# Performance work log

Measured on AMD Instinct MI355X. Metric: run time of the kernel, lower is better.

Reference implementation:

```python
import jax, jax.numpy as jnp
import numpy as np

NUM_USERS = 100000
NUM_ITEMS = 50000
EMBED_DIM = 64
NUM_LAYERS = 3
NUM_PAIRS = 2000000  # symmetrized -> 4M directed edges


def setup_inputs() -> dict:
    key = jax.random.key(0)
    k_u, k_i, k_eu, k_ei = jax.random.split(key, 4)
    # Xavier-uniform-ish embedding tables
    bound_u = float(np.sqrt(6.0 / (NUM_USERS + EMBED_DIM)))
    bound_i = float(np.sqrt(6.0 / (NUM_ITEMS + EMBED_DIM)))
    user_weight = jax.random.uniform(k_u, (NUM_USERS, EMBED_DIM), jnp.float32, -bound_u, bound_u)
    item_weight = jax.random.uniform(k_i, (NUM_ITEMS, EMBED_DIM), jnp.float32, -bound_i, bound_i)
    users = jax.random.randint(k_eu, (NUM_PAIRS,), 0, NUM_USERS)
    items = jax.random.randint(k_ei, (NUM_PAIRS,), 0, NUM_ITEMS) + NUM_USERS
    # symmetric bipartite graph: user->item and item->user
    row = jnp.concatenate([users, items])
    col = jnp.concatenate([items, users])
    edge_index = jnp.stack([row, col])  # [2, 4M]
    return {"edge_index": edge_index, "user_weight": user_weight, "item_weight": item_weight}


def _lightgcn_conv(x, row, col, num_nodes):
    # deg over target (col) nodes
    deg = jax.ops.segment_sum(jnp.ones_like(col, dtype=x.dtype), col, num_segments=num_nodes)
    deg_inv_sqrt = jnp.where(deg > 0, jax.lax.rsqrt(jnp.maximum(deg, 1)), 0.0).astype(x.dtype)
    norm = deg_inv_sqrt[row] * deg_inv_sqrt[col]          # [E]
    msg = norm[:, None] * x[row]                           # gather + scale, [E, d]
    return jax.ops.segment_sum(msg, col, num_segments=num_nodes)  # scatter-add


def reference(edge_index, user_weight, item_weight):
    num_nodes = NUM_USERS + NUM_ITEMS
    row, col = edge_index[0], edge_index[1]
    x = jnp.concatenate([user_weight, item_weight], axis=0)  # [N, d]
    acc = x
    for _ in range(NUM_LAYERS):
        x = _lightgcn_conv(x, row, col, num_nodes)
        acc = acc + x
    final = acc / (NUM_LAYERS + 1)  # mean over layer embeddings
    return final[:NUM_USERS], final[NUM_USERS:]
```

## Files before the change

kernel.cpp:

```cpp
#include <hip/hip_runtime.h>


#define MAXBUK 640
#define CHUNK 4096
#define MAXBE 12288

__device__ __forceinline__ ushort f2bf(float f) {
  union { float f; unsigned int i; } cv;
  cv.f = f;
  unsigned int u = cv.i + 0x7FFFu + ((cv.i >> 16) & 1u);
  return (ushort)(u >> 16);
}

__device__ __forceinline__ float bflo(unsigned int w) {
  union { unsigned int i; float f; } cv;
  cv.i = w << 16;
  return cv.f;
}

__device__ __forceinline__ float bfhi(unsigned int w) {
  union { unsigned int i; float f; } cv;
  cv.i = w & 0xFFFF0000u;
  return cv.f;
}

__device__ __forceinline__ int wave_incl_scan(int v) {
  int lane = threadIdx.x & 63;
#pragma unroll
  for (int off = 1; off < 64; off <<= 1) {
    int t = __shfl_up(v, off, 64);
    if (lane >= off) v += t;
  }
  return v;
}


__global__ __launch_bounds__(256) void bhist_k(const int4* __restrict__ col4, int E4,
                                               const int* __restrict__ col, int E,
                                               int* __restrict__ bcnt, int nbuk) {
  __shared__ int lc[MAXBUK];
  for (int b = threadIdx.x; b < nbuk; b += 256) lc[b] = 0;
  __syncthreads();
  int i = blockIdx.x * 256 + threadIdx.x;
  int stride = gridDim.x * 256;
  for (int j = i; j < E4; j += stride) {
    int4 c = col4[j];
    atomicAdd(&lc[c.x >> 8], 1);
    atomicAdd(&lc[c.y >> 8], 1);
    atomicAdd(&lc[c.z >> 8], 1);
    atomicAdd(&lc[c.w >> 8], 1);
  }
  for (int j = E4 * 4 + i; j < E; j += stride) atomicAdd(&lc[col[j] >> 8], 1);
  __syncthreads();
  for (int b = threadIdx.x; b < nbuk; b += 256) {
    int c = lc[b];
    if (c) atomicAdd(&bcnt[b], c);
  }
}


__global__ void bscan_k(const int* __restrict__ bcnt, int* __restrict__ boffs,
                        int* __restrict__ gcursor, ushort* __restrict__ za,
                        ushort* __restrict__ zb, int nbuk, int E, int N) {
  int tid = threadIdx.x;
  int v = (tid < nbuk) ? bcnt[tid] : 0;
  int incl = wave_incl_scan(v);
  __shared__ int wsum[16];
  int wid = tid >> 6, lane = tid & 63;
  if (lane == 63) wsum[wid] = incl;
  __syncthreads();
  if (tid == 0) {
    int run = 0;
#pragma unroll
    for (int j = 0; j < 16; ++j) { int t = wsum[j]; wsum[j] = run; run += t; }
  }
  __syncthreads();
  int excl = incl - v + wsum[wid];
  if (tid < nbuk) {
    boffs[tid] = excl;
    gcursor[tid] = excl;
  }
  if (tid == 0) boffs[nbuk] = E;
  if (tid < 64) {
    za[N * 64 + tid] = 0;
    zb[N * 64 + tid] = 0;
  }
}


__global__ __launch_bounds__(256) void part_k(
    const int* __restrict__ row, const int* __restrict__ col, int E,
    int* __restrict__ gcursor, int* __restrict__ ebk, int nbuk) {
  __shared__ int cnt[MAXBUK];
  __shared__ int start[MAXBUK];
  __shared__ int ghead[MAXBUK];
  __shared__ int ebuf[CHUNK];
  __shared__ int gofs[CHUNK];
  __shared__ int wsum[4];

  const int tid = threadIdx.x;
  const int base = blockIdx.x * CHUNK;
  const int m = min(CHUNK, E - base);

  for (int b = tid; b < nbuk; b += 256) cnt[b] = 0;
  __syncthreads();

  int rec[16];
  int bb[16];
#pragma unroll
  for (int k = 0; k < 16; ++k) {
    int idx = k * 256 + tid;
    bb[k] = -1;
    if (idx < m) {
      int i = base + idx;
      int c = col[i];
      int r = row[i];
      rec[k] = r | ((c & 255) << 18);
      bb[k] = c >> 8;
      atomicAdd(&cnt[c >> 8], 1);
    }
  }
  __syncthreads();

  const int b0 = tid * 3;
  int lc0 = (b0 + 0 < nbuk) ? cnt[b0 + 0] : 0;
  int lc1 = (b0 + 1 < nbuk) ? cnt[b0 + 1] : 0;
  int lc2 = (b0 + 2 < nbuk) ? cnt[b0 + 2] : 0;
  int s = lc0 + lc1 + lc2;
  int incl = wave_incl_scan(s);
  int wid = tid >> 6, lane = tid & 63;
  if (lane == 63) wsum[wid] = incl;
  __syncthreads();
  int wb = 0;
#pragma unroll
  for (int j = 0; j < 4; ++j)
    if (j < wid) wb += wsum[j];
  int run = incl - s + wb;
  if (b0 + 0 < nbuk) { start[b0 + 0] = run; run += lc0; }
  if (b0 + 1 < nbuk) { start[b0 + 1] = run; run += lc1; }
  if (b0 + 2 < nbuk) { start[b0 + 2] = run; run += lc2; }
  __syncthreads();

  for (int b = tid; b < nbuk; b += 256) {
    int cb = cnt[b];
    if (cb > 0) {
      int g = atomicAdd(&gcursor[b], cb);
      ghead[b] = g - start[b];
    }
  }
  __syncthreads();

#pragma unroll
  for (int k = 0; k < 16; ++k) {
    if (bb[k] >= 0) {
      int slot = atomicAdd(&start[bb[k]], 1);
      ebuf[slot] = rec[k];
      gofs[slot] = ghead[bb[k]];
    }
  }
  __syncthreads();

  for (int s2 = tid; s2 < m; s2 += 256) ebk[gofs[s2] + s2] = ebuf[s2];
}


__global__ __launch_bounds__(256) void bsort_k(
    const int* __restrict__ boffs, const int* __restrict__ ebk,
    int* __restrict__ srcs, int* __restrict__ offs,
    float* __restrict__ dis, float* __restrict__ dis2,
    const float4* __restrict__ uw4, const float4* __restrict__ iw4,
    ushort* __restrict__ za, int N, int NU, int E) {
  __shared__ int cnt[256];
  __shared__ float disv[256];
  __shared__ int wsum[4];
  __shared__ int obuf[MAXBE];
  const int tid = threadIdx.x;
  const int node0 = blockIdx.x << 8;
  const int nn = min(256, N - node0);
  const int g0 = boffs[blockIdx.x];
  const int g1 = boffs[blockIdx.x + 1];
  const int m = g1 - g0;

  cnt[tid] = 0;
  __syncthreads();
  for (int i = tid; i < m; i += 256) atomicAdd(&cnt[(ebk[g0 + i] >> 18) & 255], 1);
  __syncthreads();

  int v = cnt[tid];
  int incl = wave_incl_scan(v);
  int wid = tid >> 6, lane = tid & 63;
  if (lane == 63) wsum[wid] = incl;
  __syncthreads();
  int wb = 0;
#pragma unroll
  for (int j = 0; j < 4; ++j)
    if (j < wid) wb += wsum[j];
  int excl = incl - v + wb;

  float dv = v > 0 ? 1.0f / sqrtf((float)v) : 0.0f;
  disv[tid] = dv;
  if (tid < nn) {
    int node = node0 + tid;
    offs[node] = g0 + excl;
    dis[node] = dv;
    dis2[node] = dv * dv;
  }
  if (blockIdx.x == 0 && tid == 0) offs[N] = E;

  __syncthreads();
  cnt[tid] = excl;
  __syncthreads();

  for (int i = tid; i < m; i += 256) {
    int r = ebk[g0 + i];
    int slot = atomicAdd(&cnt[(r >> 18) & 255], 1);
    if (slot < MAXBE) obuf[slot] = r & 0x3FFFF;
  }
  __syncthreads();
  for (int i = tid; i < m; i += 256) srcs[g0 + i] = obuf[i];

  for (int g = tid; g < nn * 16; g += 256) {
    int rel = g >> 4;
    int comp = g & 15;
    int node = node0 + rel;
    float4 x = (node < NU) ? uw4[node * 16 + comp] : iw4[(node - NU) * 16 + comp];
    float d = disv[rel];
    ushort4 o;
    o.x = f2bf(x.x * d);
    o.y = f2bf(x.y * d);
    o.z = f2bf(x.z * d);
    o.w = f2bf(x.w * d);
    *reinterpret_cast<ushort4*>(&za[node * 64 + comp * 4]) = o;
  }
}


template <int LAYER>
__global__ __launch_bounds__(256) void spmm_k(
    const int* __restrict__ offs, const int* __restrict__ srcs,
    const ushort* __restrict__ zin, ushort* __restrict__ zout,
    const float* __restrict__ uw, const float* __restrict__ iw,
    const float* __restrict__ dis, const float* __restrict__ dis2,
    float* __restrict__ dout, int N, int NU) {
  int wid = blockIdx.x * 4 + (threadIdx.x >> 6);
  int lane = threadIdx.x & 63;
  if (wid >= N) return;
  int NI = N - NU;
  int n = (wid < NI) ? (NU + wid) : (wid - NI);
  n = __builtin_amdgcn_readfirstlane(n);
  int e0 = __builtin_amdgcn_readfirstlane(offs[n]);
  int e1 = __builtin_amdgcn_readfirstlane(offs[n + 1]);

  const int li = lane & 31;
  const int hi = lane >> 5;

  float ax = 0.0f, ay = 0.0f;
  for (int base = e0; base < e1; base += 64) {
    int rem = e1 - base;
    int src = (lane < rem) ? srcs[base + lane] : N;
    int kk = min(rem, 64);
    for (int j = 0; j < kk; j += 8) {
#pragma unroll
      for (int t = 0; t < 4; ++t) {
        int sA = __builtin_amdgcn_readlane(src, j + 2 * t);
        int sB = __builtin_amdgcn_readlane(src, j + 2 * t + 1);
        int s = hi ? sB : sA;
        unsigned int w32 =
            *reinterpret_cast<const unsigned int*>(&zin[(s << 6) + li * 2]);
        ax += bflo(w32);
        ay += bfhi(w32);
      }
    }
  }
  ax += __shfl_xor(ax, 32, 64);
  ay += __shfl_xor(ay, 32, 64);

  if (hi == 0) {
    float d1 = dis[n];
    int o = n * 64 + li * 2;
    float xlx = d1 * ax, xly = d1 * ay;
    if (LAYER == 1) {
      const float* xp = (n < NU) ? (uw + o) : (iw + (o - NU * 64));
      float2 x0 = *reinterpret_cast<const float2*>(xp);
      float z2 = dis2[n];
      *reinterpret_cast<ushort2*>(&zout[o]) = make_ushort2(f2bf(z2 * ax), f2bf(z2 * ay));
      *reinterpret_cast<float2*>(&dout[o]) = make_float2(x0.x + xlx, x0.y + xly);
    } else if (LAYER == 2) {
      float z2 = dis2[n];
      *reinterpret_cast<ushort2*>(&zout[o]) = make_ushort2(f2bf(z2 * ax), f2bf(z2 * ay));
      float2 dc = *reinterpret_cast<const float2*>(&dout[o]);
      *reinterpret_cast<float2*>(&dout[o]) = make_float2(dc.x + xlx, dc.y + xly);
    } else {
      float2 dc = *reinterpret_cast<const float2*>(&dout[o]);
      *reinterpret_cast<float2*>(&dout[o]) =
          make_float2((dc.x + xlx) * 0.25f, (dc.y + xly) * 0.25f);
    }
  }
}

extern "C" void kernel_launch(void* const* d_in, const int* in_sizes, int n_in,
                              void* d_out, int out_size, void* d_ws, size_t ws_size,
                              hipStream_t stream) {
  const int* edge_index = (const int*)d_in[0];
  const float* uw = (const float*)d_in[1];
  const float* iw = (const float*)d_in[2];
  const int E = in_sizes[0] / 2;
  const int NU = in_sizes[1] / 64;
  const int NI = in_sizes[2] / 64;
  const int N = NU + NI;
  const int nbuk = (N + 255) >> 8;

  const int* row = edge_index;
  const int* col = edge_index + E;

  char* w = (char*)d_ws;
  auto carve = [&](size_t bytes) {
    char* p = w;
    w += (bytes + 255) & ~(size_t)255;
    return (void*)p;
  };
  int* bcnt = (int*)carve((size_t)MAXBUK * sizeof(int));
  int* boffs = (int*)carve((size_t)(MAXBUK + 1) * sizeof(int));
  int* gcursor = (int*)carve((size_t)MAXBUK * sizeof(int));
  int* offs = (int*)carve((size_t)(N + 1) * sizeof(int));
  float* dis = (float*)carve((size_t)N * sizeof(float));
  float* dis2 = (float*)carve((size_t)N * sizeof(float));
  int* ebk = (int*)carve((size_t)E * sizeof(int));
  int* srcs = (int*)carve((size_t)E * sizeof(int));
  ushort* za = (ushort*)carve((size_t)(N + 1) * 64 * sizeof(ushort));
  ushort* zb = (ushort*)carve((size_t)(N + 1) * 64 * sizeof(ushort));

  float* out = (float*)d_out;

  (void)hipMemsetAsync(bcnt, 0, (size_t)MAXBUK * sizeof(int), stream);
  bhist_k<<<512, 256, 0, stream>>>((const int4*)col, E / 4, col, E, bcnt, nbuk);
  bscan_k<<<1, 1024, 0, stream>>>(bcnt, boffs, gcursor, za, zb, nbuk, E, N);
  part_k<<<(E + CHUNK - 1) / CHUNK, 256, 0, stream>>>(row, col, E, gcursor, ebk, nbuk);
  bsort_k<<<nbuk, 256, 0, stream>>>(boffs, ebk, srcs, offs, dis, dis2,
                                    (const float4*)uw, (const float4*)iw, za, N, NU, E);

  int sb = (N + 3) / 4;
  spmm_k<1><<<sb, 256, 0, stream>>>(offs, srcs, za, zb, uw, iw, dis, dis2, out, N, NU);
  spmm_k<2><<<sb, 256, 0, stream>>>(offs, srcs, zb, za, uw, iw, dis, dis2, out, N, NU);
  spmm_k<3><<<sb, 256, 0, stream>>>(offs, srcs, za, zb, uw, iw, dis, dis2, out, N, NU);
}
```

Measured before the change: 412.8 us.

## Gather 8 neighbor rows per wave with 16-byte loads and prefetch next batch

The SpMM kernel now splits each wave into 8 groups of 8 lanes. Each lane loads 16 bytes (8 bf16 values), so one wave instruction fetches 8 neighbor rows, where the old code fetched 2 rows with 4-byte loads. The next batch's row is software-prefetched while the current one is accumulated, and a 3-step xor-shuffle tree reduces the 8 partial sums. This targets fewer, wider memory instructions and more memory-level parallelism in the gather, at the cost of 8 accumulators plus extra shuffles per node.

```diff
diff --git a/kernel.cpp b/kernel.cpp
--- a/kernel.cpp
+++ b/kernel.cpp
@@ -22,6 +22,10 @@
   union { unsigned int i; float f; } cv;
   cv.i = w & 0xFFFF0000u;
   return cv.f;
+}
+
+__device__ __forceinline__ unsigned int packbf(float lo, float hi) {
+  return (unsigned int)f2bf(lo) | ((unsigned int)f2bf(hi) << 16);
 }
 
 __device__ __forceinline__ int wave_incl_scan(int v) {
@@ -251,50 +255,78 @@
   int e0 = __builtin_amdgcn_readfirstlane(offs[n]);
   int e1 = __builtin_amdgcn_readfirstlane(offs[n + 1]);
 
-  const int li = lane & 31;
-  const int hi = lane >> 5;
-
-  float ax = 0.0f, ay = 0.0f;
+  const int g = lane >> 3;
+  const int dimb = (lane & 7) * 8;
+
+  float a0 = 0.f, a1 = 0.f, a2 = 0.f, a3 = 0.f,
+        a4 = 0.f, a5 = 0.f, a6 = 0.f, a7 = 0.f;
+
   for (int base = e0; base < e1; base += 64) {
     int rem = e1 - base;
     int src = (lane < rem) ? srcs[base + lane] : N;
     int kk = min(rem, 64);
+    int s0 = __shfl(src, g, 64);
+    uint4 w = *reinterpret_cast<const uint4*>(zin + ((long)s0 << 6) + dimb);
     for (int j = 0; j < kk; j += 8) {
-#pragma unroll
-      for (int t = 0; t < 4; ++t) {
-        int sA = __builtin_amdgcn_readlane(src, j + 2 * t);
-        int sB = __builtin_amdgcn_readlane(src, j + 2 * t + 1);
-        int s = hi ? sB : sA;
-        unsigned int w32 =
-            *reinterpret_cast<const unsigned int*>(&zin[(s << 6) + li * 2]);
-        ax += bflo(w32);
-        ay += bfhi(w32);
+      uint4 wn;
+      const bool more = (j + 8) < kk;
+      if (more) {
+        int sn = __shfl(src, j + 8 + g, 64);
+        wn = *reinterpret_cast<const uint4*>(zin + ((long)sn << 6) + dimb);
       }
-    }
-  }
-  ax += __shfl_xor(ax, 32, 64);
-  ay += __shfl_xor(ay, 32, 64);
-
-  if (hi == 0) {
+      a0 += bflo(w.x); a1 += bfhi(w.x);
+      a2 += bflo(w.y); a3 += bfhi(w.y);
+      a4 += bflo(w.z); a5 += bfhi(w.z);
+      a6 += bflo(w.w); a7 += bfhi(w.w);
+      if (more) w = wn;
+    }
+  }
+
+#pragma unroll
+  for (int off = 8; off < 64; off <<= 1) {
+    a0 += __shfl_xor(a0, off, 64);
+    a1 += __shfl_xor(a1, off, 64);
+    a2 += __shfl_xor(a2, off, 64);
+    a3 += __shfl_xor(a3, off, 64);
+    a4 += __shfl_xor(a4, off, 64);
+    a5 += __shfl_xor(a5, off, 64);
+    a6 += __shfl_xor(a6, off, 64);
+    a7 += __shfl_xor(a7, off, 64);
+  }
+
+  if (lane < 8) {
+    int o = n * 64 + lane * 8;
     float d1 = dis[n];
-    int o = n * 64 + li * 2;
-    float xlx = d1 * ax, xly = d1 * ay;
+    if (LAYER == 1 || LAYER == 2) {
+      float z2 = dis2[n];
+      uint4 zo;
+      zo.x = packbf(z2 * a0, z2 * a1);
+      zo.y = packbf(z2 * a2, z2 * a3);
+      zo.z = packbf(z2 * a4, z2 * a5);
+      zo.w = packbf(z2 * a6, z2 * a7);
+      *reinterpret_cast<uint4*>(&zout[o]) = zo;
+    }
+    float4 dlo, dhi;
+    dlo.x = d1 * a0; dlo.y = d1 * a1; dlo.z = d1 * a2; dlo.w = d1 * a3;
+    dhi.x = d1 * a4; dhi.y = d1 * a5; dhi.z = d1 * a6; dhi.w = d1 * a7;
     if (LAYER == 1) {
       const float* xp = (n < NU) ? (uw + o) : (iw + (o - NU * 64));
-      float2 x0 = *reinterpret_cast<const float2*>(xp);
-      float z2 = dis2[n];
-      *reinterpret_cast<ushort2*>(&zout[o]) = make_ushort2(f2bf(z2 * ax), f2bf(z2 * ay));
-      *reinterpret_cast<float2*>(&dout[o]) = make_float2(x0.x + xlx, x0.y + xly);
-    } else if (LAYER == 2) {
-      float z2 = dis2[n];
-      *reinterpret_cast<ushort2*>(&zout[o]) = make_ushort2(f2bf(z2 * ax), f2bf(z2 * ay));
-      float2 dc = *reinterpret_cast<const float2*>(&dout[o]);
-      *reinterpret_cast<float2*>(&dout[o]) = make_float2(dc.x + xlx, dc.y + xly);
+      float4 xa = *reinterpret_cast<const float4*>(xp);
+      float4 xb = *reinterpret_cast<const float4*>(xp + 4);
+      dlo.x += xa.x; dlo.y += xa.y; dlo.z += xa.z; dlo.w += xa.w;
+      dhi.x += xb.x; dhi.y += xb.y; dhi.z += xb.z; dhi.w += xb.w;
     } else {
-      float2 dc = *reinterpret_cast<const float2*>(&dout[o]);
-      *reinterpret_cast<float2*>(&dout[o]) =
-          make_float2((dc.x + xlx) * 0.25f, (dc.y + xly) * 0.25f);
-    }
+      float4 ca = *reinterpret_cast<const float4*>(&dout[o]);
+      float4 cb = *reinterpret_cast<const float4*>(&dout[o + 4]);
+      dlo.x += ca.x; dlo.y += ca.y; dlo.z += ca.z; dlo.w += ca.w;
+      dhi.x += cb.x; dhi.y += cb.y; dhi.z += cb.z; dhi.w += cb.w;
+      if (LAYER == 3) {
+        dlo.x *= 0.25f; dlo.y *= 0.25f; dlo.z *= 0.25f; dlo.w *= 0.25f;
+        dhi.x *= 0.25f; dhi.y *= 0.25f; dhi.z *= 0.25f; dhi.w *= 0.25f;
+      }
+    }
+    *reinterpret_cast<float4*>(&dout[o]) = dlo;
+    *reinterpret_cast<float4*>(&dout[o + 4]) = dhi;
   }
 }
 
```

After: 416.3 us. No clear change (+0.8%).
